# Optimization experiments

Measured on AMD Instinct MI355X. Metric: run time of the kernel, lower is better.

The kernel has to match this reference:

```python
import jax, jax.numpy as jnp
import numpy as np

N = 500_000
IN_CH = 64
OUT_CH = 32
HEADS = 4
NUM_SEGS = 1024


def setup_inputs() -> dict:
    key = jax.random.key(0)
    ks = jax.random.split(key, 8)
    x = jax.random.normal(ks[0], (N, IN_CH), dtype=jnp.float32)
    batch = jnp.sort(jax.random.randint(ks[1], (N,), 0, NUM_SEGS, dtype=jnp.int32))
    batch = batch.at[-1].set(NUM_SEGS - 1)  # mimic size = batch[-1]+1 == NUM_SEGS
    s_in = 1.0 / np.sqrt(IN_CH)
    s_hg = 1.0 / np.sqrt(HEADS * IN_CH)
    s_hm = 1.0 / np.sqrt(OUT_CH * HEADS)
    # gate_nn: Linear(in, heads*in, bias=False) -> PReLU -> Linear(heads*in, heads, bias=False)
    gate_w1 = jax.random.uniform(ks[2], (HEADS * IN_CH, IN_CH), jnp.float32, -s_in, s_in)
    prelu_a = jnp.asarray(0.25, dtype=jnp.float32)
    gate_w2 = jax.random.uniform(ks[3], (HEADS, HEADS * IN_CH), jnp.float32, -s_hg, s_hg)
    # nn: Linear(in, out*heads) -> ReLU -> Linear(out*heads, out*heads)
    mlp_w1 = jax.random.uniform(ks[4], (OUT_CH * HEADS, IN_CH), jnp.float32, -s_in, s_in)
    mlp_b1 = jax.random.uniform(ks[5], (OUT_CH * HEADS,), jnp.float32, -s_in, s_in)
    mlp_w2 = jax.random.uniform(ks[6], (OUT_CH * HEADS, OUT_CH * HEADS), jnp.float32, -s_hm, s_hm)
    mlp_b2 = jax.random.uniform(ks[7], (OUT_CH * HEADS,), jnp.float32, -s_hm, s_hm)
    return {"x": x, "batch": batch, "num_segments": NUM_SEGS,
            "gate_w1": gate_w1, "prelu_a": prelu_a, "gate_w2": gate_w2,
            "mlp_w1": mlp_w1, "mlp_b1": mlp_b1, "mlp_w2": mlp_w2, "mlp_b2": mlp_b2}


def reference(x, batch, num_segments, gate_w1, prelu_a, gate_w2,
              mlp_w1, mlp_b1, mlp_w2, mlp_b2):
    n = x.shape[0]
    # gate network: [N, heads]
    h = x @ gate_w1.T
    h = jnp.where(h >= 0, h, prelu_a * h)  # PReLU (shared scalar slope)
    gate = h @ gate_w2.T
    # feature MLP: [N, heads, out]
    feat = jax.nn.relu(x @ mlp_w1.T + mlp_b1) @ mlp_w2.T + mlp_b2
    feat = feat.reshape(n, HEADS, -1)
    # segment (per-graph) softmax over nodes, per head
    gmax = jax.ops.segment_max(gate, batch, num_segments=num_segments)  # [S, heads]
    escore = jnp.exp(gate - gmax[batch])
    denom = jax.ops.segment_sum(escore, batch, num_segments=num_segments)
    score = escore / (denom[batch] + 1e-16)  # [N, heads]
    # weighted scatter-add pooling
    out = jax.ops.segment_sum(score[..., None] * feat, batch, num_segments=num_segments)
    return out.reshape(num_segments, -1)  # [S, heads*out]
```

## Files before the change

### kernel.cpp

```cpp
#include <hip/hip_runtime.h>
#include <cstdint>
#include <cstddef>

#define NN 500000
#define NTILES 31250
#define NG 7813
#define NBLK 1024
#define NWAVES (NBLK * 2)

typedef __attribute__((ext_vector_type(8))) short short8;
typedef __attribute__((ext_vector_type(4))) float floatx4;
typedef __attribute__((ext_vector_type(4))) float fv4;

__device__ __forceinline__ unsigned short f2bf(float f) {
  union { float f; unsigned u; } v; v.f = f;
  unsigned r = v.u + 0x7FFFu + ((v.u >> 16) & 1u);
  return (unsigned short)(r >> 16);
}
__device__ __forceinline__ unsigned pack2bf(float a, float b) {
  return (unsigned)f2bf(a) | ((unsigned)f2bf(b) << 16);
}
__device__ __forceinline__ fv4 ntload4(const float* p) {
  return __builtin_nontemporal_load((const fv4*)p);
}

#define MFMA16(a, b, c) __builtin_amdgcn_mfma_f32_16x16x32_bf16((a), (b), (c), 0, 0, 0)

__global__ void swizzle_weights(const float* __restrict__ gw1, const float* __restrict__ mw1,
                                const float* __restrict__ mw2,
                                unsigned short* __restrict__ gw1s,
                                unsigned short* __restrict__ mw1s,
                                unsigned short* __restrict__ mw2s) {
  int e = blockIdx.x * 256 + threadIdx.x;
  const float* src; unsigned short* dst; int ksteps, K, local;
  if (e < 16384)      { src = gw1; dst = gw1s; ksteps = 2; K = 64;  local = e; }
  else if (e < 24576) { src = mw1; dst = mw1s; ksteps = 2; K = 64;  local = e - 16384; }
  else                { src = mw2; dst = mw2s; ksteps = 4; K = 128; local = e - 24576; }
  int j = local & 7, lane = (local >> 3) & 63, tile = local >> 9;
  int ks = tile % ksteps, mtile = tile / ksteps;
  int row = mtile * 16 + (lane & 15);
  int k   = ks * 32 + ((lane >> 4) & 3) * 8 + j;
  dst[local] = f2bf(src[row * K + k]);
}

#define FLUSH() do {                                                          \
  _Pragma("unroll") for (int mt_ = 0; mt_ < 8; ++mt_) {                       \
    _Pragma("unroll") for (int r_ = 0; r_ < 4; ++r_) {                        \
      float v_ = acc[mt_][r_];                                                \
      v_ += __shfl_xor(v_, 1); v_ += __shfl_xor(v_, 2);                       \
      v_ += __shfl_xor(v_, 4); v_ += __shfl_xor(v_, 8);                       \
      if (lcol == 0)                                                          \
        atomicAdd(&out[cur_seg * 128 + mt_ * 16 + quad * 4 + r_], v_);        \
      acc[mt_][r_] = 0.f; } }                                                 \
  _Pragma("unroll") for (int h_ = 0; h_ < 4; ++h_) {                          \
    float v_ = e_sum[h_];                                                     \
    v_ += __shfl_xor(v_, 1); v_ += __shfl_xor(v_, 2);                         \
    v_ += __shfl_xor(v_, 4); v_ += __shfl_xor(v_, 8);                         \
    if (lane == 0) atomicAdd(&denom[cur_seg * 4 + h_], v_);                   \
    e_sum[h_] = 0.f; }                                                        \
} while (0)

__global__ __launch_bounds__(128, 2) void fused_kernel(
    const float* __restrict__ x, const int* __restrict__ batch,
    const unsigned short* __restrict__ gw1s, const unsigned short* __restrict__ mw1s,
    const unsigned short* __restrict__ mw2s, const float* __restrict__ gw2,
    const float* __restrict__ prelu_a, const float* __restrict__ b1,
    float* __restrict__ denom, float* __restrict__ out) {
  __shared__ float gw2L[1024];
  __shared__ unsigned short hs_all[2][64 * 132];
  const int t = threadIdx.x;
  const int wave = t >> 6, lane = t & 63;
  const int quad = lane >> 4, lcol = lane & 15;
  unsigned short* hs = hs_all[wave];

  for (int i = t; i < 1024; i += 128) gw2L[i] = gw2[(i & 3) * 256 + (i >> 2)];
  __syncthreads();

  const float slope = prelu_a[0];
  const int W = blockIdx.x * 2 + wave;
  const int g0 = (int)(((long long)W * NG) / NWAVES);
  const int g1 = (int)(((long long)(W + 1) * NG) / NWAVES);

  float acc[8][4];
  float e_sum[4] = {0.f, 0.f, 0.f, 0.f};
#pragma unroll
  for (int mt = 0; mt < 8; ++mt)
#pragma unroll
    for (int r = 0; r < 4; ++r) acc[mt][r] = 0.f;
  int fs = g0 * 64; if (fs > NN - 1) fs = NN - 1;
  int cur_seg = batch[fs];

  for (int g = g0; g < g1; ++g) {
    const int base = g * 64;
    int sv[4]; float emask[4];
    short8 bx[4][2];
#pragma unroll
    for (int nt = 0; nt < 4; ++nt) {
      int tb = base + nt * 16;
      bool ok = tb < NN;
      int node = ok ? (tb + lcol) : (NN - 1);
      emask[nt] = ok ? 1.f : 0.f;
      sv[nt] = batch[node];
      const float* xp = x + (size_t)node * 64 + quad * 8;
      fv4 v0 = ntload4(xp), v1 = ntload4(xp + 4);
      fv4 v2 = ntload4(xp + 32), v3 = ntload4(xp + 36);
      union { short8 s; unsigned u[4]; } u0, u1;
      u0.u[0] = pack2bf(v0[0], v0[1]); u0.u[1] = pack2bf(v0[2], v0[3]);
      u0.u[2] = pack2bf(v1[0], v1[1]); u0.u[3] = pack2bf(v1[2], v1[3]);
      u1.u[0] = pack2bf(v2[0], v2[1]); u1.u[1] = pack2bf(v2[2], v2[3]);
      u1.u[2] = pack2bf(v3[0], v3[1]); u1.u[3] = pack2bf(v3[2], v3[3]);
      bx[nt][0] = u0.s; bx[nt][1] = u1.s;
    }

    float gp[4][4];
#pragma unroll
    for (int nt = 0; nt < 4; ++nt)
#pragma unroll
      for (int h = 0; h < 4; ++h) gp[nt][h] = 0.f;
#pragma unroll 2
    for (int mt = 0; mt < 16; ++mt) {
      short8 a0 = *(const short8*)(gw1s + ((size_t)(mt * 2 + 0) * 64 + lane) * 8);
      short8 a1 = *(const short8*)(gw1s + ((size_t)(mt * 2 + 1) * 64 + lane) * 8);
      fv4 g2r0 = *(const fv4*)&gw2L[(mt * 16 + quad * 4 + 0) * 4];
      fv4 g2r1 = *(const fv4*)&gw2L[(mt * 16 + quad * 4 + 1) * 4];
      fv4 g2r2 = *(const fv4*)&gw2L[(mt * 16 + quad * 4 + 2) * 4];
      fv4 g2r3 = *(const fv4*)&gw2L[(mt * 16 + quad * 4 + 3) * 4];
#pragma unroll
      for (int nt = 0; nt < 4; ++nt) {
        floatx4 cc = {0.f, 0.f, 0.f, 0.f};
        cc = MFMA16(a0, bx[nt][0], cc);
        cc = MFMA16(a1, bx[nt][1], cc);
        float h0 = cc[0] >= 0.f ? cc[0] : slope * cc[0];
        float h1v = cc[1] >= 0.f ? cc[1] : slope * cc[1];
        float h2 = cc[2] >= 0.f ? cc[2] : slope * cc[2];
        float h3 = cc[3] >= 0.f ? cc[3] : slope * cc[3];
        gp[nt][0] += g2r0[0]*h0 + g2r1[0]*h1v + g2r2[0]*h2 + g2r3[0]*h3;
        gp[nt][1] += g2r0[1]*h0 + g2r1[1]*h1v + g2r2[1]*h2 + g2r3[1]*h3;
        gp[nt][2] += g2r0[2]*h0 + g2r1[2]*h1v + g2r2[2]*h2 + g2r3[2]*h3;
        gp[nt][3] += g2r0[3]*h0 + g2r1[3]*h1v + g2r2[3]*h2 + g2r3[3]*h3;
      }
    }
    float e16[4][4];
#pragma unroll
    for (int nt = 0; nt < 4; ++nt)
#pragma unroll
      for (int h = 0; h < 4; ++h) {
        float v = gp[nt][h];
        v += __shfl_xor(v, 16);
        v += __shfl_xor(v, 32);
        e16[nt][h] = __expf(v) * emask[nt];
      }

#pragma unroll 2
    for (int mt = 0; mt < 8; ++mt) {
      short8 a0 = *(const short8*)(mw1s + ((size_t)(mt * 2 + 0) * 64 + lane) * 8);
      short8 a1 = *(const short8*)(mw1s + ((size_t)(mt * 2 + 1) * 64 + lane) * 8);
      fv4 bias = *(const fv4*)(b1 + mt * 16 + quad * 4);
#pragma unroll
      for (int nt = 0; nt < 4; ++nt) {
        floatx4 cc = {0.f, 0.f, 0.f, 0.f};
        cc = MFMA16(a0, bx[nt][0], cc);
        cc = MFMA16(a1, bx[nt][1], cc);
        uint2 p;
        p.x = pack2bf(fmaxf(cc[0] + bias[0], 0.f), fmaxf(cc[1] + bias[1], 0.f));
        p.y = pack2bf(fmaxf(cc[2] + bias[2], 0.f), fmaxf(cc[3] + bias[3], 0.f));
        *(uint2*)(hs + (nt * 16 + lcol) * 132 + mt * 16 + quad * 4) = p;
      }
    }
    union BH { short8 s; uint2 u[2]; } bh[4][4];
#pragma unroll
    for (int nt = 0; nt < 4; ++nt)
#pragma unroll
      for (int ks = 0; ks < 4; ++ks) {
        const unsigned short* hp = hs + (nt * 16 + lcol) * 132 + ks * 32 + quad * 8;
        bh[nt][ks].u[0] = *(const uint2*)hp;
        bh[nt][ks].u[1] = *(const uint2*)(hp + 4);
      }

    int p = 0;
    while (p < 64) {
      int pn = p >> 4, pl = p & 15;
      int sel = (pn == 0) ? sv[0] : (pn == 1) ? sv[1] : (pn == 2) ? sv[2] : sv[3];
      int s = __shfl(sel, pl);
      if (s != cur_seg) { FLUSH(); cur_seg = s; }
      int cnt = 0;
      float em[4][4];
#pragma unroll
      for (int nt = 0; nt < 4; ++nt) {
        bool mm = (sv[nt] == s);
        cnt += (int)__popcll(__ballot(mm));
        float m = mm ? 1.f : 0.f;
#pragma unroll
        for (int h = 0; h < 4; ++h) em[nt][h] = e16[nt][h] * m;
      }
#pragma unroll
      for (int h = 0; h < 4; ++h)
        e_sum[h] += em[0][h] + em[1][h] + em[2][h] + em[3][h];
#pragma unroll
      for (int mt = 0; mt < 8; ++mt) {
        short8 a20 = *(const short8*)(mw2s + ((size_t)(mt * 4 + 0) * 64 + lane) * 8);
        short8 a21 = *(const short8*)(mw2s + ((size_t)(mt * 4 + 1) * 64 + lane) * 8);
        short8 a22 = *(const short8*)(mw2s + ((size_t)(mt * 4 + 2) * 64 + lane) * 8);
        short8 a23 = *(const short8*)(mw2s + ((size_t)(mt * 4 + 3) * 64 + lane) * 8);
        const int hh = mt >> 1;
#pragma unroll
        for (int nt = 0; nt < 4; ++nt) {
          floatx4 cc = {0.f, 0.f, 0.f, 0.f};
          cc = MFMA16(a20, bh[nt][0].s, cc);
          cc = MFMA16(a21, bh[nt][1].s, cc);
          cc = MFMA16(a22, bh[nt][2].s, cc);
          cc = MFMA16(a23, bh[nt][3].s, cc);
          float e = em[nt][hh];
          acc[mt][0] = fmaf(e, cc[0], acc[mt][0]);
          acc[mt][1] = fmaf(e, cc[1], acc[mt][1]);
          acc[mt][2] = fmaf(e, cc[2], acc[mt][2]);
          acc[mt][3] = fmaf(e, cc[3], acc[mt][3]);
        }
      }
      p += (cnt >> 2);
    }
  }
  FLUSH();
}

__global__ void finalize_kernel(float* __restrict__ out, const float* __restrict__ denom,
                                const float* __restrict__ b2) {
  int i = blockIdx.x * 256 + threadIdx.x;
  int seg = i >> 7, head = (i >> 5) & 3;
  float d = denom[seg * 4 + head];
  out[i] = (d > 0.f) ? (out[i] / d + b2[i & 127]) : 0.f;
}

extern "C" void kernel_launch(void* const* d_in, const int* in_sizes, int n_in,
                              void* d_out, int out_size, void* d_ws, size_t ws_size,
                              hipStream_t stream) {
  const float* x     = (const float*)d_in[0];
  const int*   batch = (const int*)d_in[1];
  const float* gw1 = (const float*)d_in[3];
  const float* pa  = (const float*)d_in[4];
  const float* gw2 = (const float*)d_in[5];
  const float* mw1 = (const float*)d_in[6];
  const float* mb1 = (const float*)d_in[7];
  const float* mw2 = (const float*)d_in[8];
  const float* mb2 = (const float*)d_in[9];
  float* out = (float*)d_out;

  char* ws = (char*)d_ws;
  float* denom = (float*)ws;
  unsigned short* gw1s = (unsigned short*)(ws + 16384);
  unsigned short* mw1s = (unsigned short*)(ws + 49152);
  unsigned short* mw2s = (unsigned short*)(ws + 65536);

  hipMemsetAsync(denom, 0, 4096 * sizeof(float), stream);
  hipMemsetAsync(out, 0, (size_t)out_size * sizeof(float), stream);

  swizzle_weights<<<160, 256, 0, stream>>>(gw1, mw1, mw2, gw1s, mw1s, mw2s);

  fused_kernel<<<NBLK, 128, 0, stream>>>(x, batch, gw1s, mw1s, mw2s, gw2,
                                         pa, mb1, denom, out);

  finalize_kernel<<<512, 256, 0, stream>>>(out, denom, mb2);
}
```

Before: 305.0 us.

## Keep MLP hidden in registers and compute gate second layer via MFMA

Lays out the first-layer MFMA accumulators so they feed the next MFMA directly as B operands, removing the LDS round-trip for the hidden activations. The gate's second linear layer now runs on MFMA against a padded, swizzled bf16 copy of gw2 instead of scalar FMAs over an LDS table, followed by a lane shuffle. It also switches to a cheaper bf16 pack (add plus byte permute, round-half-up rather than round-to-nearest-even) and reshapes the launch to 256-thread blocks with 4 waves each. The trade-offs are bf16 rounding of the PReLU outputs before the gate matmul, and higher register pressure under the new launch bounds.

```diff
diff --git a/kernel.cpp b/kernel.cpp
--- a/kernel.cpp
+++ b/kernel.cpp
@@ -3,10 +3,9 @@
 #include <cstddef>
 
 #define NN 500000
-#define NTILES 31250
 #define NG 7813
-#define NBLK 1024
-#define NWAVES (NBLK * 2)
+#define NBLK 768
+#define NWAVES (NBLK * 4)
 
 typedef __attribute__((ext_vector_type(8))) short short8;
 typedef __attribute__((ext_vector_type(4))) float floatx4;
@@ -17,8 +16,10 @@
   unsigned r = v.u + 0x7FFFu + ((v.u >> 16) & 1u);
   return (unsigned short)(r >> 16);
 }
-__device__ __forceinline__ unsigned pack2bf(float a, float b) {
-  return (unsigned)f2bf(a) | ((unsigned)f2bf(b) << 16);
+__device__ __forceinline__ unsigned packbf2(float a, float b) {
+  unsigned ua = __float_as_uint(a) + 0x8000u;
+  unsigned ub = __float_as_uint(b) + 0x8000u;
+  return __builtin_amdgcn_perm(ub, ua, 0x07060302u);
 }
 __device__ __forceinline__ fv4 ntload4(const float* p) {
   return __builtin_nontemporal_load((const fv4*)p);
@@ -26,21 +27,30 @@
 
 #define MFMA16(a, b, c) __builtin_amdgcn_mfma_f32_16x16x32_bf16((a), (b), (c), 0, 0, 0)
 
-__global__ void swizzle_weights(const float* __restrict__ gw1, const float* __restrict__ mw1,
-                                const float* __restrict__ mw2,
-                                unsigned short* __restrict__ gw1s,
-                                unsigned short* __restrict__ mw1s,
-                                unsigned short* __restrict__ mw2s) {
+__global__ void swizzle_weights(const float* __restrict__ gw1, const float* __restrict__ gw2,
+                                const float* __restrict__ mw1, const float* __restrict__ mw2,
+                                unsigned short* __restrict__ gw1s, unsigned short* __restrict__ gw2s,
+                                unsigned short* __restrict__ mw1s, unsigned short* __restrict__ mw2s) {
   int e = blockIdx.x * 256 + threadIdx.x;
-  const float* src; unsigned short* dst; int ksteps, K, local;
-  if (e < 16384)      { src = gw1; dst = gw1s; ksteps = 2; K = 64;  local = e; }
-  else if (e < 24576) { src = mw1; dst = mw1s; ksteps = 2; K = 64;  local = e - 16384; }
-  else                { src = mw2; dst = mw2s; ksteps = 4; K = 128; local = e - 24576; }
-  int j = local & 7, lane = (local >> 3) & 63, tile = local >> 9;
-  int ks = tile % ksteps, mtile = tile / ksteps;
-  int row = mtile * 16 + (lane & 15);
-  int k   = ks * 32 + ((lane >> 4) & 3) * 8 + j;
-  dst[local] = f2bf(src[row * K + k]);
+  if (e < 16384) {
+    int local = e, j = local & 7, lane = (local >> 3) & 63, tile = local >> 9;
+    int ks = tile & 1, mt = tile >> 1, q = (lane >> 4) & 3;
+    gw1s[local] = f2bf(gw1[(mt * 16 + (lane & 15)) * 64 + ks * 32 + q * 8 + j]);
+  } else if (e < 20480) {
+    int local = e - 16384, j = local & 7, lane = (local >> 3) & 63, b = local >> 9;
+    int q = (lane >> 4) & 3, head = lane & 15;
+    int wcol = b * 32 + (j < 4 ? q * 4 + j : 16 + q * 4 + (j - 4));
+    gw2s[local] = (head < 4) ? f2bf(gw2[head * 256 + wcol]) : (unsigned short)0;
+  } else if (e < 28672) {
+    int local = e - 20480, j = local & 7, lane = (local >> 3) & 63, tile = local >> 9;
+    int ks = tile & 1, mt = tile >> 1, q = (lane >> 4) & 3;
+    mw1s[local] = f2bf(mw1[(mt * 16 + (lane & 15)) * 64 + ks * 32 + q * 8 + j]);
+  } else {
+    int local = e - 28672, j = local & 7, lane = (local >> 3) & 63, tile = local >> 9;
+    int ks = tile & 3, mt = tile >> 2, q = (lane >> 4) & 3;
+    int hidx = ks * 32 + (j < 4 ? q * 4 + j : 16 + q * 4 + (j - 4));
+    mw2s[local] = f2bf(mw2[(mt * 16 + (lane & 15)) * 128 + hidx]);
+  }
 }
 
 #define FLUSH() do {                                                          \
@@ -60,24 +70,18 @@
     e_sum[h_] = 0.f; }                                                        \
 } while (0)
 
-__global__ __launch_bounds__(128, 2) void fused_kernel(
+__global__ __launch_bounds__(256, 3) void fused_kernel(
     const float* __restrict__ x, const int* __restrict__ batch,
-    const unsigned short* __restrict__ gw1s, const unsigned short* __restrict__ mw1s,
-    const unsigned short* __restrict__ mw2s, const float* __restrict__ gw2,
+    const unsigned short* __restrict__ gw1s, const unsigned short* __restrict__ gw2s,
+    const unsigned short* __restrict__ mw1s, const unsigned short* __restrict__ mw2s,
     const float* __restrict__ prelu_a, const float* __restrict__ b1,
     float* __restrict__ denom, float* __restrict__ out) {
-  __shared__ float gw2L[1024];
-  __shared__ unsigned short hs_all[2][64 * 132];
   const int t = threadIdx.x;
   const int wave = t >> 6, lane = t & 63;
   const int quad = lane >> 4, lcol = lane & 15;
-  unsigned short* hs = hs_all[wave];
-
-  for (int i = t; i < 1024; i += 128) gw2L[i] = gw2[(i & 3) * 256 + (i >> 2)];
-  __syncthreads();
-
   const float slope = prelu_a[0];
-  const int W = blockIdx.x * 2 + wave;
+
+  const int W = blockIdx.x * 4 + wave;
   const int g0 = (int)(((long long)W * NG) / NWAVES);
   const int g1 = (int)(((long long)(W + 1) * NG) / NWAVES);
 
@@ -87,8 +91,7 @@
   for (int mt = 0; mt < 8; ++mt)
 #pragma unroll
     for (int r = 0; r < 4; ++r) acc[mt][r] = 0.f;
-  int fs = g0 * 64; if (fs > NN - 1) fs = NN - 1;
-  int cur_seg = batch[fs];
+  int cur_seg = batch[g0 * 64];
 
   for (int g = g0; g < g1; ++g) {
     const int base = g * 64;
@@ -105,77 +108,69 @@
       fv4 v0 = ntload4(xp), v1 = ntload4(xp + 4);
       fv4 v2 = ntload4(xp + 32), v3 = ntload4(xp + 36);
       union { short8 s; unsigned u[4]; } u0, u1;
-      u0.u[0] = pack2bf(v0[0], v0[1]); u0.u[1] = pack2bf(v0[2], v0[3]);
-      u0.u[2] = pack2bf(v1[0], v1[1]); u0.u[3] = pack2bf(v1[2], v1[3]);
-      u1.u[0] = pack2bf(v2[0], v2[1]); u1.u[1] = pack2bf(v2[2], v2[3]);
-      u1.u[2] = pack2bf(v3[0], v3[1]); u1.u[3] = pack2bf(v3[2], v3[3]);
+      u0.u[0] = packbf2(v0[0], v0[1]); u0.u[1] = packbf2(v0[2], v0[3]);
+      u0.u[2] = packbf2(v1[0], v1[1]); u0.u[3] = packbf2(v1[2], v1[3]);
+      u1.u[0] = packbf2(v2[0], v2[1]); u1.u[1] = packbf2(v2[2], v2[3]);
+      u1.u[2] = packbf2(v3[0], v3[1]); u1.u[3] = packbf2(v3[2], v3[3]);
       bx[nt][0] = u0.s; bx[nt][1] = u1.s;
     }
 
-    float gp[4][4];
+    floatx4 c2[4];
+#pragma unroll
+    for (int nt = 0; nt < 4; ++nt) c2[nt] = (floatx4){0.f, 0.f, 0.f, 0.f};
+#pragma unroll 2
+    for (int b = 0; b < 8; ++b) {
+      const unsigned short* g1p = gw1s + (size_t)b * 2048;
+      short8 a00 = *(const short8*)(g1p + lane * 8);
+      short8 a01 = *(const short8*)(g1p + 512 + lane * 8);
+      short8 a10 = *(const short8*)(g1p + 1024 + lane * 8);
+      short8 a11 = *(const short8*)(g1p + 1536 + lane * 8);
+      short8 g2a = *(const short8*)(gw2s + (size_t)b * 512 + lane * 8);
+#pragma unroll
+      for (int nt = 0; nt < 4; ++nt) {
+        floatx4 cA = {0.f, 0.f, 0.f, 0.f}, cB = {0.f, 0.f, 0.f, 0.f};
+        cA = MFMA16(a00, bx[nt][0], cA); cA = MFMA16(a01, bx[nt][1], cA);
+        cB = MFMA16(a10, bx[nt][0], cB); cB = MFMA16(a11, bx[nt][1], cB);
+        union { short8 s; unsigned u[4]; } bf;
+        bf.u[0] = packbf2(fmaxf(cA[0], slope * cA[0]), fmaxf(cA[1], slope * cA[1]));
+        bf.u[1] = packbf2(fmaxf(cA[2], slope * cA[2]), fmaxf(cA[3], slope * cA[3]));
+        bf.u[2] = packbf2(fmaxf(cB[0], slope * cB[0]), fmaxf(cB[1], slope * cB[1]));
+        bf.u[3] = packbf2(fmaxf(cB[2], slope * cB[2]), fmaxf(cB[3], slope * cB[3]));
+        c2[nt] = MFMA16(g2a, bf.s, c2[nt]);
+      }
+    }
+    float e16[4][4];
 #pragma unroll
     for (int nt = 0; nt < 4; ++nt)
 #pragma unroll
-      for (int h = 0; h < 4; ++h) gp[nt][h] = 0.f;
+      for (int h = 0; h < 4; ++h) {
+        float gv = __shfl(c2[nt][h], lcol);
+        e16[nt][h] = __expf(gv) * emask[nt];
+      }
+
+    short8 bh[4][4];
+#pragma unroll
+    for (int nt = 0; nt < 4; ++nt) {
 #pragma unroll 2
-    for (int mt = 0; mt < 16; ++mt) {
-      short8 a0 = *(const short8*)(gw1s + ((size_t)(mt * 2 + 0) * 64 + lane) * 8);
-      short8 a1 = *(const short8*)(gw1s + ((size_t)(mt * 2 + 1) * 64 + lane) * 8);
-      fv4 g2r0 = *(const fv4*)&gw2L[(mt * 16 + quad * 4 + 0) * 4];
-      fv4 g2r1 = *(const fv4*)&gw2L[(mt * 16 + quad * 4 + 1) * 4];
-      fv4 g2r2 = *(const fv4*)&gw2L[(mt * 16 + quad * 4 + 2) * 4];
-      fv4 g2r3 = *(const fv4*)&gw2L[(mt * 16 + quad * 4 + 3) * 4];
-#pragma unroll
-      for (int nt = 0; nt < 4; ++nt) {
-        floatx4 cc = {0.f, 0.f, 0.f, 0.f};
-        cc = MFMA16(a0, bx[nt][0], cc);
-        cc = MFMA16(a1, bx[nt][1], cc);
-        float h0 = cc[0] >= 0.f ? cc[0] : slope * cc[0];
-        float h1v = cc[1] >= 0.f ? cc[1] : slope * cc[1];
-        float h2 = cc[2] >= 0.f ? cc[2] : slope * cc[2];
-        float h3 = cc[3] >= 0.f ? cc[3] : slope * cc[3];
-        gp[nt][0] += g2r0[0]*h0 + g2r1[0]*h1v + g2r2[0]*h2 + g2r3[0]*h3;
-        gp[nt][1] += g2r0[1]*h0 + g2r1[1]*h1v + g2r2[1]*h2 + g2r3[1]*h3;
-        gp[nt][2] += g2r0[2]*h0 + g2r1[2]*h1v + g2r2[2]*h2 + g2r3[2]*h3;
-        gp[nt][3] += g2r0[3]*h0 + g2r1[3]*h1v + g2r2[3]*h2 + g2r3[3]*h3;
-      }
-    }
-    float e16[4][4];
-#pragma unroll
-    for (int nt = 0; nt < 4; ++nt)
-#pragma unroll
-      for (int h = 0; h < 4; ++h) {
-        float v = gp[nt][h];
-        v += __shfl_xor(v, 16);
-        v += __shfl_xor(v, 32);
-        e16[nt][h] = __expf(v) * emask[nt];
-      }
-
-#pragma unroll 2
-    for (int mt = 0; mt < 8; ++mt) {
-      short8 a0 = *(const short8*)(mw1s + ((size_t)(mt * 2 + 0) * 64 + lane) * 8);
-      short8 a1 = *(const short8*)(mw1s + ((size_t)(mt * 2 + 1) * 64 + lane) * 8);
-      fv4 bias = *(const fv4*)(b1 + mt * 16 + quad * 4);
-#pragma unroll
-      for (int nt = 0; nt < 4; ++nt) {
-        floatx4 cc = {0.f, 0.f, 0.f, 0.f};
-        cc = MFMA16(a0, bx[nt][0], cc);
-        cc = MFMA16(a1, bx[nt][1], cc);
-        uint2 p;
-        p.x = pack2bf(fmaxf(cc[0] + bias[0], 0.f), fmaxf(cc[1] + bias[1], 0.f));
-        p.y = pack2bf(fmaxf(cc[2] + bias[2], 0.f), fmaxf(cc[3] + bias[3], 0.f));
-        *(uint2*)(hs + (nt * 16 + lcol) * 132 + mt * 16 + quad * 4) = p;
-      }
-    }
-    union BH { short8 s; uint2 u[2]; } bh[4][4];
-#pragma unroll
-    for (int nt = 0; nt < 4; ++nt)
-#pragma unroll
-      for (int ks = 0; ks < 4; ++ks) {
-        const unsigned short* hp = hs + (nt * 16 + lcol) * 132 + ks * 32 + quad * 8;
-        bh[nt][ks].u[0] = *(const uint2*)hp;
-        bh[nt][ks].u[1] = *(const uint2*)(hp + 4);
-      }
+      for (int b = 0; b < 4; ++b) {
+        const unsigned short* m1p = mw1s + (size_t)b * 2048;
+        short8 a00 = *(const short8*)(m1p + lane * 8);
+        short8 a01 = *(const short8*)(m1p + 512 + lane * 8);
+        short8 a10 = *(const short8*)(m1p + 1024 + lane * 8);
+        short8 a11 = *(const short8*)(m1p + 1536 + lane * 8);
+        fv4 biasA = *(const fv4*)(b1 + b * 32 + quad * 4);
+        fv4 biasB = *(const fv4*)(b1 + b * 32 + 16 + quad * 4);
+        floatx4 cA = {0.f, 0.f, 0.f, 0.f}, cB = {0.f, 0.f, 0.f, 0.f};
+        cA = MFMA16(a00, bx[nt][0], cA); cA = MFMA16(a01, bx[nt][1], cA);
+        cB = MFMA16(a10, bx[nt][0], cB); cB = MFMA16(a11, bx[nt][1], cB);
+        union { short8 s; unsigned u[4]; } bf;
+        bf.u[0] = packbf2(fmaxf(cA[0] + biasA[0], 0.f), fmaxf(cA[1] + biasA[1], 0.f));
+        bf.u[1] = packbf2(fmaxf(cA[2] + biasA[2], 0.f), fmaxf(cA[3] + biasA[3], 0.f));
+        bf.u[2] = packbf2(fmaxf(cB[0] + biasB[0], 0.f), fmaxf(cB[1] + biasB[1], 0.f));
+        bf.u[3] = packbf2(fmaxf(cB[2] + biasB[2], 0.f), fmaxf(cB[3] + biasB[3], 0.f));
+        bh[nt][b] = bf.s;
+      }
+    }
 
     int p = 0;
     while (p < 64) {
@@ -198,18 +193,19 @@
         e_sum[h] += em[0][h] + em[1][h] + em[2][h] + em[3][h];
 #pragma unroll
       for (int mt = 0; mt < 8; ++mt) {
-        short8 a20 = *(const short8*)(mw2s + ((size_t)(mt * 4 + 0) * 64 + lane) * 8);
-        short8 a21 = *(const short8*)(mw2s + ((size_t)(mt * 4 + 1) * 64 + lane) * 8);
-        short8 a22 = *(const short8*)(mw2s + ((size_t)(mt * 4 + 2) * 64 + lane) * 8);
-        short8 a23 = *(const short8*)(mw2s + ((size_t)(mt * 4 + 3) * 64 + lane) * 8);
+        const unsigned short* m2p = mw2s + (size_t)mt * 2048;
+        short8 a20 = *(const short8*)(m2p + lane * 8);
+        short8 a21 = *(const short8*)(m2p + 512 + lane * 8);
+        short8 a22 = *(const short8*)(m2p + 1024 + lane * 8);
+        short8 a23 = *(const short8*)(m2p + 1536 + lane * 8);
         const int hh = mt >> 1;
 #pragma unroll
         for (int nt = 0; nt < 4; ++nt) {
           floatx4 cc = {0.f, 0.f, 0.f, 0.f};
-          cc = MFMA16(a20, bh[nt][0].s, cc);
-          cc = MFMA16(a21, bh[nt][1].s, cc);
-          cc = MFMA16(a22, bh[nt][2].s, cc);
-          cc = MFMA16(a23, bh[nt][3].s, cc);
+          cc = MFMA16(a20, bh[nt][0], cc);
+          cc = MFMA16(a21, bh[nt][1], cc);
+          cc = MFMA16(a22, bh[nt][2], cc);
+          cc = MFMA16(a23, bh[nt][3], cc);
           float e = em[nt][hh];
           acc[mt][0] = fmaf(e, cc[0], acc[mt][0]);
           acc[mt][1] = fmaf(e, cc[1], acc[mt][1]);
@@ -248,15 +244,17 @@
   char* ws = (char*)d_ws;
   float* denom = (float*)ws;
   unsigned short* gw1s = (unsigned short*)(ws + 16384);
-  unsigned short* mw1s = (unsigned short*)(ws + 49152);
-  unsigned short* mw2s = (unsigned short*)(ws + 65536);
+  unsigned short* gw2s = (unsigned short*)(ws + 49152);
+  unsigned short* mw1s = (unsigned short*)(ws + 57344);
+  unsigned short* mw2s = (unsigned short*)(ws + 73728);
 
   hipMemsetAsync(denom, 0, 4096 * sizeof(float), stream);
   hipMemsetAsync(out, 0, (size_t)out_size * sizeof(float), stream);
 
-  swizzle_weights<<<160, 256, 0, stream>>>(gw1, mw1, mw2, gw1s, mw1s, mw2s);
-
-  fused_kernel<<<NBLK, 128, 0, stream>>>(x, batch, gw1s, mw1s, mw2s, gw2,
+  swizzle_weights<<<176, 256, 0, stream>>>(gw1, gw2, mw1, mw2,
+                                           gw1s, gw2s, mw1s, mw2s);
+
+  fused_kernel<<<NBLK, 256, 0, stream>>>(x, batch, gw1s, gw2s, mw1s, mw2s,
                                          pa, mb1, denom, out);
 
   finalize_kernel<<<512, 256, 0, stream>>>(out, denom, mb2);
```

New measurement: 360.1 us. 18.1% more time.
